# Optimization experiments

Hardware: AMD Instinct MI355X
Metric: run time of the kernel (lower is better)

## Reference

```python
import jax, jax.numpy as jnp
import numpy as np

B, L, C = 8, 4096, 256
H = 8            # num_heads
D = C // H       # head_dim = 32
CHUNK = 128


def _build_slopes(n):
    # ALiBi slopes for power-of-2 n: 2^(-8/n * (i+1)); cast fp16 like the torch module
    s = np.array([2.0 ** (-(8.0 / n) * (i + 1)) for i in range(n)], dtype=np.float32)
    return jnp.asarray(s.astype(np.float16).astype(np.float32))  # [H]


def setup_inputs() -> dict:
    key = jax.random.key(0)
    ks = jax.random.split(key, 6)
    x = jax.random.normal(ks[0], (B, L, C), dtype=jnp.float32)
    rel_pos = jax.random.normal(ks[1], (1, L, C), dtype=jnp.float32) * 0.02  # trunc_normal std=0.02
    qkv_w = jax.random.normal(ks[2], (3 * C, C), dtype=jnp.float32) * (C ** -0.5)
    q_gamma = jnp.ones((H, 1, D), dtype=jnp.float32) / (D ** 0.5)
    k_gamma = jnp.ones((H, 1, D), dtype=jnp.float32) / (D ** 0.5)
    proj_w = jax.random.normal(ks[3], (C, C), dtype=jnp.float32) * (C ** -0.5)
    proj_b = jnp.zeros((C,), dtype=jnp.float32)
    return {"x": x, "rel_pos": rel_pos, "qkv_w": qkv_w, "q_gamma": q_gamma,
            "k_gamma": k_gamma, "proj_w": proj_w, "proj_b": proj_b}


def _rms_norm(t, gamma):
    # t: [B,H,L,D]; gamma: [H,1,D]. F.normalize(dim=-1) then * sqrt(D) * gamma
    n = jnp.sqrt(jnp.sum(t * t, axis=-1, keepdims=True))
    t = t / jnp.maximum(n, 1e-12)
    return t * (D ** 0.5) * gamma[None]


def _lightning_attn(q, k, v, slopes):
    # q,k,v: [B,H,L,D]; slopes: [H]. o_t = sum_{s<=t} exp(-slope*(t-s)) (q_t.k_s) v_s
    nc = L // CHUNK
    c = CHUNK
    qc = q.reshape(B, H, nc, c, D)
    kc = k.reshape(B, H, nc, c, D)
    vc = v.reshape(B, H, nc, c, D)

    idx = jnp.arange(c, dtype=jnp.float32)
    diff = idx[:, None] - idx[None, :]                       # [c,c]
    s = slopes[:, None, None]                                # [H,1,1]
    mask = jnp.where(diff >= 0, jnp.exp(-s * diff), 0.0)     # [H,c,c]

    # intra-chunk: [B,H,nc,c,c]
    scores = jnp.einsum("bhncd,bhnmd->bhncm", qc, kc) * mask[None, :, None]
    o_intra = jnp.einsum("bhncm,bhnmd->bhncd", scores, vc)

    # inter-chunk recurrence over decayed KV state [B,H,D,D]
    q_decay = jnp.exp(-slopes[:, None] * idx[None, :])[None, :, :, None]        # [1,H,c,1]
    k_decay = jnp.exp(-slopes[:, None] * (c - idx[None, :]))[None, :, :, None]  # [1,H,c,1]
    blk_decay = jnp.exp(-slopes * c)[:, None, None]                             # [H,1,1]

    def step(kv, inp):
        qi, ki, vi = inp                                   # each [B,H,c,D]
        o = jnp.einsum("bhcd,bhde->bhce", qi * q_decay, kv)
        kv = blk_decay * kv + jnp.einsum("bhcd,bhce->bhde", ki * k_decay, vi)
        return kv, o

    kv0 = jnp.zeros((B, H, D, D), dtype=q.dtype)
    qs = jnp.moveaxis(qc, 2, 0)  # [nc,B,H,c,D]
    ks_ = jnp.moveaxis(kc, 2, 0)
    vs = jnp.moveaxis(vc, 2, 0)
    _, o_inter = jax.lax.scan(step, kv0, (qs, ks_, vs))    # [nc,B,H,c,D]
    o_inter = jnp.moveaxis(o_inter, 0, 2)                  # [B,H,nc,c,D]

    return (o_intra + o_inter).reshape(B, H, L, D)


def reference(x, rel_pos, qkv_w, q_gamma, k_gamma, proj_w, proj_b):
    slopes = _build_slopes(H)
    h = x + rel_pos                                        # [B,L,C]
    qkv = h @ qkv_w.T                                      # [B,L,3C]
    qkv = qkv.reshape(B, L, 3, H, D).transpose(2, 0, 3, 1, 4)  # [3,B,H,L,D]
    q, k, v = qkv[0], qkv[1], qkv[2]
    q = q * (D ** -0.5)            # no-op through normalize, kept for fidelity
    q = _rms_norm(q, q_gamma)
    k = _rms_norm(k, k_gamma)
    o = _lightning_attn(q, k, v, slopes)                   # [B,H,L,D]
    o = o.transpose(0, 2, 1, 3).reshape(B, L, C)
    return o @ proj_w.T + proj_b
```

## Files before the change

kernel.cpp:

```cpp
#include <hip/hip_runtime.h>
#include <hip/hip_bf16.h>

#define B_ 8
#define L_ 4096
#define C_ 256
#define H_ 8
#define D_ 32
#define CHUNK_ 128
#define NC_ 32
#define M_ (B_*L_)

typedef _Float16 f16x8 __attribute__((ext_vector_type(8)));
typedef _Float16 f16x4 __attribute__((ext_vector_type(4)));
typedef float    f32x4 __attribute__((ext_vector_type(4)));

#define GLOAD_LDS16(g, l) __builtin_amdgcn_global_load_lds( \
    (const __attribute__((address_space(1))) unsigned int*)(g), \
    (__attribute__((address_space(3))) unsigned int*)(l), 16, 0, 0)

__global__ __launch_bounds__(256) void k_cast_w(
    const float* __restrict__ qw, const float* __restrict__ pw,
    _Float16* __restrict__ qwb, _Float16* __restrict__ pwb)
{
    const int i = (blockIdx.x * 256 + threadIdx.x) * 4;
    const float* src; _Float16* dst; int off;
    if (i < 768 * 256) { src = qw; dst = qwb; off = i; }
    else               { src = pw; dst = pwb; off = i - 768 * 256; }
    float4 v = *(const float4*)(src + off);
    f16x4 o = { (_Float16)v.x, (_Float16)v.y, (_Float16)v.z, (_Float16)v.w };
    *(f16x4*)(dst + off) = o;
}

__global__ __launch_bounds__(256) void k_qkv_fused(
    const float* __restrict__ x, const float* __restrict__ rel,
    const _Float16* __restrict__ Bw,
    const float* __restrict__ qg, const float* __restrict__ kg,
    _Float16* __restrict__ Qg, _Float16* __restrict__ Kg, _Float16* __restrict__ Vtg)
{
    __shared__ _Float16 As[128 * 32];
    __shared__ _Float16 Bs[128 * 32];
    __shared__ _Float16 Ws[128 * 132];
    const int tid = threadIdx.x;
    const int wv = tid >> 6, ln = tid & 63;
    const int m0 = blockIdx.y * 128;
    const int n0 = blockIdx.x * 128;
    const int lr = ln >> 2;
    const int lc = (ln & 3) * 8;
    const int wm = (wv >> 1) * 64;
    const int wn = (wv & 1) * 64;
    const int fr = ln & 15;
    const int fk = (ln >> 4) * 8;

    f32x4 acc[4][4] = {};
    const _Float16* gb = Bw + (size_t)(n0 + wv * 16 + lr) * 256 + lc;

    for (int k0 = 0; k0 < 256; k0 += 32) {
        GLOAD_LDS16(gb + k0,            Bs + (wv * 16) * 32);
        GLOAD_LDS16(gb + k0 + 64 * 256, Bs + (64 + wv * 16) * 32);
#pragma unroll
        for (int t = 0; t < 4; ++t) {
            const int flat = t * 256 + tid;
            const int row = flat >> 3;
            const int c4  = (flat & 7) * 4;
            const float* xp = x   + (size_t)(m0 + row) * 256 + k0 + c4;
            const float* rp = rel + (size_t)((m0 + row) & 4095) * 256 + k0 + c4;
            float4 xv = *(const float4*)xp;
            float4 rv = *(const float4*)rp;
            f16x4 hv = { (_Float16)(xv.x + rv.x), (_Float16)(xv.y + rv.y),
                         (_Float16)(xv.z + rv.z), (_Float16)(xv.w + rv.w) };
            *(f16x4*)(As + row * 32 + c4) = hv;
        }
        __syncthreads();
        f16x8 af[4], bf[4];
#pragma unroll
        for (int i = 0; i < 4; ++i)
            af[i] = *(const f16x8*)(As + (wm + i * 16 + fr) * 32 + fk);
#pragma unroll
        for (int j = 0; j < 4; ++j)
            bf[j] = *(const f16x8*)(Bs + (wn + j * 16 + fr) * 32 + fk);
#pragma unroll
        for (int i = 0; i < 4; ++i)
#pragma unroll
            for (int j = 0; j < 4; ++j)
                acc[i][j] = __builtin_amdgcn_mfma_f32_16x16x32_f16(
                    af[i], bf[j], acc[i][j], 0, 0, 0);
        __syncthreads();
    }

    const int cr = (ln >> 4) * 4;
    const int cc = ln & 15;
    const int kind = n0 >> 8;
    const int col0 = (n0 & 255) + wn;
    const int bb   = m0 >> 12;
    const int l00  = m0 & 4095;

    if (kind < 2) {
        const float* gsrc = kind ? kg : qg;
        float gma[2][2];
#pragma unroll
        for (int jp = 0; jp < 2; ++jp)
#pragma unroll
            for (int jj = 0; jj < 2; ++jj)
                gma[jp][jj] = gsrc[((col0 >> 5) + jp) * 32 + jj * 16 + cc];
#pragma unroll
        for (int i = 0; i < 4; ++i)
#pragma unroll
            for (int r = 0; r < 4; ++r) {
                const int irow = wm + i * 16 + cr + r;
#pragma unroll
                for (int jp = 0; jp < 2; ++jp) {
                    const float a0 = acc[i][jp * 2][r];
                    const float a1 = acc[i][jp * 2 + 1][r];
                    float ss = a0 * a0 + a1 * a1;
                    ss += __shfl_xor(ss, 1);
                    ss += __shfl_xor(ss, 2);
                    ss += __shfl_xor(ss, 4);
                    ss += __shfl_xor(ss, 8);
                    const float sc = 5.656854249492381f / fmaxf(sqrtf(ss), 1e-12f);
                    Ws[irow * 132 + wn + jp * 32 + cc]      = (_Float16)(a0 * sc * gma[jp][0]);
                    Ws[irow * 132 + wn + jp * 32 + 16 + cc] = (_Float16)(a1 * sc * gma[jp][1]);
                }
            }
        __syncthreads();
        _Float16* P = kind ? Kg : Qg;
        const int hbase = (n0 & 255) >> 5;
#pragma unroll
        for (int kk = 0; kk < 8; ++kk) {
            const int c = kk * 256 + tid;
            const int hh = c >> 9;
            const int rr = (c >> 2) & 127;
            const int part = (c & 3) * 8;
            f16x8 v8 = *(const f16x8*)(Ws + rr * 132 + hh * 32 + part);
            *(f16x8*)(P + ((size_t)(bb * 8 + hbase + hh) * 4096 + l00 + rr) * 32 + part) = v8;
        }
    } else {
#pragma unroll
        for (int i = 0; i < 4; ++i)
#pragma unroll
            for (int j = 0; j < 4; ++j) {
                const int col = col0 + j * 16 + cc;
                const int hh = col >> 5, e = col & 31;
                const int l0 = l00 + wm + i * 16 + cr;
                f16x4 v4 = { (_Float16)acc[i][j][0], (_Float16)acc[i][j][1],
                             (_Float16)acc[i][j][2], (_Float16)acc[i][j][3] };
                *(f16x4*)(Vtg + ((size_t)(bb * 8 + hh) * 32 + e) * 4096 + l0) = v4;
            }
    }
}

__global__ __launch_bounds__(256) void k_chunk_kv(
    const _Float16* __restrict__ Kg, const _Float16* __restrict__ Vtg,
    float* __restrict__ kvbuf)
{
    __shared__ float ks[128 * 32];
    __shared__ float vst[32 * 129];
    const int blk = blockIdx.x;
    const int n  = blk & 31;
    const int bh = blk >> 5;
    const int h  = bh & 7;
    const float slope = exp2f(-(float)(h + 1));
    const float sl2 = slope * 1.44269504f;
    const int tid = threadIdx.x;
    const _Float16* Kc = Kg + ((size_t)bh * 4096 + n * CHUNK_) * 32;
#pragma unroll
    for (int i = 0; i < 2; ++i) {
        int flat = i * 256 + tid;
        int pos = flat >> 2;
        int d0  = (flat & 3) * 8;
        f16x8 k8 = *(const f16x8*)(Kc + flat * 8);
        float kd = exp2f(-sl2 * (float)(CHUNK_ - pos));
#pragma unroll
        for (int j = 0; j < 8; ++j) ks[pos * 32 + d0 + j] = (float)k8[j] * kd;
        int e = flat >> 4;
        int seg = flat & 15;
        f16x8 v8 = *(const f16x8*)(Vtg + ((size_t)bh * 32 + e) * 4096 + n * CHUNK_ + seg * 8);
#pragma unroll
        for (int j = 0; j < 8; ++j) vst[e * 129 + seg * 8 + j] = (float)v8[j];
    }
    __syncthreads();
    const int e   = tid & 31;
    const int dd0 = tid >> 5;
    float acc[4] = {0.f, 0.f, 0.f, 0.f};
    for (int pos = 0; pos < CHUNK_; ++pos) {
        float vv = vst[e * 129 + pos];
        acc[0] += ks[pos * 32 + dd0 +  0] * vv;
        acc[1] += ks[pos * 32 + dd0 +  8] * vv;
        acc[2] += ks[pos * 32 + dd0 + 16] * vv;
        acc[3] += ks[pos * 32 + dd0 + 24] * vv;
    }
    float* out = kvbuf + (size_t)blk * 1024;
#pragma unroll
    for (int i = 0; i < 4; ++i) out[(dd0 + i * 8) * 32 + e] = acc[i];
}

__global__ __launch_bounds__(256) void k_scan(float* __restrict__ kvbuf)
{
    const int bh = blockIdx.x;
    const int tid = threadIdx.x;
    const float slope = exp2f(-(float)((bh & 7) + 1));
    const float bd = __expf(-slope * (float)CHUNK_);
    float4 st = {0.f, 0.f, 0.f, 0.f};
    float4* base = (float4*)(kvbuf + (size_t)bh * NC_ * 1024) + tid;
#pragma unroll
    for (int g = 0; g < 4; ++g) {
        float4 tmp[8];
#pragma unroll
        for (int k = 0; k < 8; ++k) tmp[k] = base[(g * 8 + k) * 256];
#pragma unroll
        for (int k = 0; k < 8; ++k) {
            base[(g * 8 + k) * 256] = st;
            st.x = bd * st.x + tmp[k].x;
            st.y = bd * st.y + tmp[k].y;
            st.z = bd * st.z + tmp[k].z;
            st.w = bd * st.w + tmp[k].w;
        }
    }
}

__global__ __launch_bounds__(256) void k_attn(
    const _Float16* __restrict__ Qg, const _Float16* __restrict__ Kg,
    const _Float16* __restrict__ Vtg, const float* __restrict__ kvbuf,
    _Float16* __restrict__ attnp)
{
    __shared__ _Float16 Qs[128 * 32];
    __shared__ _Float16 Ks[128 * 32];
    __shared__ _Float16 Vt[32 * 136];
    __shared__ _Float16 KVt[32 * 40];
    __shared__ _Float16 Ss[128 * 136];
    __shared__ _Float16 Os[128 * 36];
    __shared__ float ejs[CHUNK_];
    const int blk = blockIdx.x;
    const int n  = blk & 31;
    const int bh = blk >> 5;
    const int h  = bh & 7;
    const float slope = exp2f(-(float)(h + 1));
    const float sl2 = slope * 1.44269504f;
    const int tid = threadIdx.x;
    const int wv = tid >> 6, ln = tid & 63;

    const _Float16* Qc = Qg + ((size_t)bh * 4096 + n * CHUNK_) * 32;
    const _Float16* Kc = Kg + ((size_t)bh * 4096 + n * CHUNK_) * 32;
#pragma unroll
    for (int i = 0; i < 2; ++i) {
        GLOAD_LDS16(Qc + (wv * 128 + i * 64 + ln) * 8, Qs + (wv * 128 + i * 64) * 8);
        GLOAD_LDS16(Kc + (wv * 128 + i * 64 + ln) * 8, Ks + (wv * 128 + i * 64) * 8);
    }
#pragma unroll
    for (int i = 0; i < 2; ++i) {
        int flat = i * 256 + tid;
        int e = flat >> 4, seg = flat & 15;
        f16x8 v8 = *(const f16x8*)(Vtg + ((size_t)bh * 32 + e) * 4096 + n * CHUNK_ + seg * 8);
        *(f16x8*)(Vt + e * 136 + seg * 8) = v8;
    }
    {
        int e = tid & 31, dg = tid >> 5;
        const float* kvp = kvbuf + (size_t)blk * 1024;
        f16x4 kv4 = { (_Float16)kvp[(dg * 4 + 0) * 32 + e],
                      (_Float16)kvp[(dg * 4 + 1) * 32 + e],
                      (_Float16)kvp[(dg * 4 + 2) * 32 + e],
                      (_Float16)kvp[(dg * 4 + 3) * 32 + e] };
        *(f16x4*)(KVt + e * 40 + dg * 4) = kv4;
    }
    if (tid < CHUNK_) ejs[tid] = exp2f(sl2 * (float)tid);
    __syncthreads();

    const int fr = ln & 15, fk = (ln >> 4) * 8;
    const int cr = (ln >> 4) * 4, cc = ln & 15;

    f16x8 aq[2];
#pragma unroll
    for (int i = 0; i < 2; ++i)
        aq[i] = *(const f16x8*)(Qs + (wv * 32 + i * 16 + fr) * 32 + fk);

    f32x4 sacc[2][8] = {};
#pragma unroll
    for (int j = 0; j < 8; ++j) {
        f16x8 bk = *(const f16x8*)(Ks + (j * 16 + fr) * 32 + fk);
#pragma unroll
        for (int i = 0; i < 2; ++i)
            sacc[i][j] = __builtin_amdgcn_mfma_f32_16x16x32_f16(aq[i], bk, sacc[i][j], 0, 0, 0);
    }
    f32x4 iacc[2][2] = {};
#pragma unroll
    for (int ct = 0; ct < 2; ++ct) {
        f16x8 bkv = *(const f16x8*)(KVt + (ct * 16 + fr) * 40 + fk);
#pragma unroll
        for (int i = 0; i < 2; ++i)
            iacc[i][ct] = __builtin_amdgcn_mfma_f32_16x16x32_f16(aq[i], bkv, iacc[i][ct], 0, 0, 0);
    }
    float ejr[8];
#pragma unroll
    for (int j = 0; j < 8; ++j) ejr[j] = ejs[j * 16 + cc];
    const float c1 = exp2f(-sl2);
    float qd_save[2][4];
#pragma unroll
    for (int i = 0; i < 2; ++i) {
        float er = exp2f(-sl2 * (float)(wv * 32 + i * 16 + cr));
#pragma unroll
        for (int r = 0; r < 4; ++r) {
            const int irow = wv * 32 + i * 16 + cr + r;
            qd_save[i][r] = er;
#pragma unroll
            for (int j = 0; j < 8; ++j) {
                const int jcol = j * 16 + cc;
                const float w = (jcol <= irow) ? ejr[j] * er : 0.f;
                Ss[irow * 136 + jcol] = (_Float16)(sacc[i][j][r] * w);
            }
            er *= c1;
        }
    }
    __syncthreads();

    f32x4 oacc[2][2] = {};
#pragma unroll
    for (int k = 0; k < 4; ++k) {
        f16x8 as[2], bv[2];
#pragma unroll
        for (int i = 0; i < 2; ++i)
            as[i] = *(const f16x8*)(Ss + (wv * 32 + i * 16 + fr) * 136 + k * 32 + fk);
#pragma unroll
        for (int ct = 0; ct < 2; ++ct)
            bv[ct] = *(const f16x8*)(Vt + (ct * 16 + fr) * 136 + k * 32 + fk);
#pragma unroll
        for (int i = 0; i < 2; ++i)
#pragma unroll
            for (int ct = 0; ct < 2; ++ct)
                oacc[i][ct] = __builtin_amdgcn_mfma_f32_16x16x32_f16(as[i], bv[ct], oacc[i][ct], 0, 0, 0);
    }
#pragma unroll
    for (int i = 0; i < 2; ++i)
#pragma unroll
        for (int r = 0; r < 4; ++r) {
            const int irow = wv * 32 + i * 16 + cr + r;
            const float qd = qd_save[i][r];
            Os[irow * 36 + cc]      = (_Float16)(oacc[i][0][r] + qd * iacc[i][0][r]);
            Os[irow * 36 + 16 + cc] = (_Float16)(oacc[i][1][r] + qd * iacc[i][1][r]);
        }
    __syncthreads();
    _Float16* abase = attnp + ((size_t)bh * 4096 + n * CHUNK_) * 32;
#pragma unroll
    for (int kk = 0; kk < 2; ++kk) {
        const int c = kk * 256 + tid;
        const int rr = c >> 2;
        const int part = (c & 3) * 8;
        *(f16x8*)(abase + rr * 32 + part) = *(const f16x8*)(Os + rr * 36 + part);
    }
}

__global__ __launch_bounds__(256) void k_proj_gemm(
    const _Float16* __restrict__ attnp, const _Float16* __restrict__ Bw,
    const float* __restrict__ bias, float* __restrict__ Cc)
{
    __shared__ _Float16 As[128 * 32];
    __shared__ _Float16 Bs[128 * 32];
    const int tid = threadIdx.x;
    const int wv = tid >> 6, ln = tid & 63;
    const int m0 = blockIdx.y * 128;
    const int n0 = blockIdx.x * 128;
    const int lr = ln >> 2;
    const int lc = (ln & 3) * 8;
    const int wm = (wv >> 1) * 64;
    const int wn = (wv & 1) * 64;
    const int fr = ln & 15;
    const int fk = (ln >> 4) * 8;

    f32x4 acc[4][4] = {};
    const int gmrow = m0 + wv * 16 + lr;
    const _Float16* ga = attnp +
        ((size_t)(gmrow >> 12) * 8 * 4096 + (gmrow & 4095)) * 32 + lc;
    const _Float16* gb = Bw + (size_t)(n0 + wv * 16 + lr) * 256 + lc;

    for (int k0 = 0; k0 < 256; k0 += 32) {
        const size_t hoff = (size_t)(k0 >> 5) * (4096 * 32);
        GLOAD_LDS16(ga + hoff,           As + (wv * 16) * 32);
        GLOAD_LDS16(ga + hoff + 64 * 32, As + (64 + wv * 16) * 32);
        GLOAD_LDS16(gb + k0,             Bs + (wv * 16) * 32);
        GLOAD_LDS16(gb + k0 + 64 * 256,  Bs + (64 + wv * 16) * 32);
        __syncthreads();
        f16x8 af[4], bf[4];
#pragma unroll
        for (int i = 0; i < 4; ++i)
            af[i] = *(const f16x8*)(As + (wm + i * 16 + fr) * 32 + fk);
#pragma unroll
        for (int j = 0; j < 4; ++j)
            bf[j] = *(const f16x8*)(Bs + (wn + j * 16 + fr) * 32 + fk);
#pragma unroll
        for (int i = 0; i < 4; ++i)
#pragma unroll
            for (int j = 0; j < 4; ++j)
                acc[i][j] = __builtin_amdgcn_mfma_f32_16x16x32_f16(
                    af[i], bf[j], acc[i][j], 0, 0, 0);
        __syncthreads();
    }
    const int cr = (ln >> 4) * 4;
    const int cc = ln & 15;
#pragma unroll
    for (int i = 0; i < 4; ++i)
#pragma unroll
        for (int j = 0; j < 4; ++j) {
            const int row = m0 + wm + i * 16 + cr;
            const int col = n0 + wn + j * 16 + cc;
            float* cp = Cc + (size_t)row * 256 + col;
            const float bb = bias[col];
#pragma unroll
            for (int r = 0; r < 4; ++r) cp[(size_t)r * 256] = acc[i][j][r] + bb;
        }
}

extern "C" void kernel_launch(void* const* d_in, const int* in_sizes, int n_in,
                              void* d_out, int out_size, void* d_ws, size_t ws_size,
                              hipStream_t stream)
{
    const float* x     = (const float*)d_in[0];
    const float* rel   = (const float*)d_in[1];
    const float* qkv_w = (const float*)d_in[2];
    const float* qg    = (const float*)d_in[3];
    const float* kg    = (const float*)d_in[4];
    const float* pw    = (const float*)d_in[5];
    const float* pb    = (const float*)d_in[6];
    float* out = (float*)d_out;
    char* wsb = (char*)d_ws;

    float*    kvb   = (float*)wsb;
    _Float16* Qg    = (_Float16*)(wsb + ((size_t)8  << 20));
    _Float16* Kg    = (_Float16*)(wsb + ((size_t)24 << 20));
    _Float16* Vtg   = (_Float16*)(wsb + ((size_t)40 << 20));
    _Float16* attnp = (_Float16*)(wsb + ((size_t)56 << 20));
    _Float16* qwb   = (_Float16*)(wsb + ((size_t)72 << 20));
    _Float16* pwb   = (_Float16*)(wsb + ((size_t)73 << 20));

    k_cast_w<<<256, 256, 0, stream>>>(qkv_w, pw, qwb, pwb);
    k_qkv_fused<<<dim3(6, 256), 256, 0, stream>>>(x, rel, qwb, qg, kg, Qg, Kg, Vtg);
    k_chunk_kv<<<2048, 256, 0, stream>>>(Kg, Vtg, kvb);
    k_scan<<<64, 256, 0, stream>>>(kvb);
    k_attn<<<2048, 256, 0, stream>>>(Qg, Kg, Vtg, kvb, attnp);
    k_proj_gemm<<<dim3(2, 256), 256, 0, stream>>>(attnp, pwb, pb, out);
}
```

Baseline: 204.9 us.

## Widen QKV GEMM tile to 128x256 with 512 threads, revectorize chunk KV

The QKV projection kernel now computes a full 256-column slice (one of q/k/v) per block with 8 waves, so each x+rel tile is loaded and converted once per kind instead of twice. Shared memory is aliased between the staging buffers and the output staging buffer, and the normalized output is written one head pair at a time with extra barriers. The chunk KV kernel transposes V in LDS so each thread accumulates a float4 of outputs with vector LDS reads and a vector store. The risks are the extra syncs in the epilogue and possible register pressure at 512 threads.

```diff
diff --git a/kernel.cpp b/kernel.cpp
--- a/kernel.cpp
+++ b/kernel.cpp
@@ -31,116 +31,110 @@
     *(f16x4*)(dst + off) = o;
 }
 
-__global__ __launch_bounds__(256) void k_qkv_fused(
+__global__ __launch_bounds__(512) void k_qkv_fused(
     const float* __restrict__ x, const float* __restrict__ rel,
     const _Float16* __restrict__ Bw,
     const float* __restrict__ qg, const float* __restrict__ kg,
     _Float16* __restrict__ Qg, _Float16* __restrict__ Kg, _Float16* __restrict__ Vtg)
 {
-    __shared__ _Float16 As[128 * 32];
-    __shared__ _Float16 Bs[128 * 32];
-    __shared__ _Float16 Ws[128 * 132];
+    __shared__ __align__(16) char smem[24576];
+    _Float16* As = (_Float16*)smem;
+    _Float16* Bs = As + 128 * 32;
+    _Float16* Ws = (_Float16*)smem;
+
     const int tid = threadIdx.x;
     const int wv = tid >> 6, ln = tid & 63;
+    const int kind = blockIdx.x;
     const int m0 = blockIdx.y * 128;
-    const int n0 = blockIdx.x * 128;
-    const int lr = ln >> 2;
-    const int lc = (ln & 3) * 8;
-    const int wm = (wv >> 1) * 64;
-    const int wn = (wv & 1) * 64;
-    const int fr = ln & 15;
-    const int fk = (ln >> 4) * 8;
-
-    f32x4 acc[4][4] = {};
-    const _Float16* gb = Bw + (size_t)(n0 + wv * 16 + lr) * 256 + lc;
-
+    const int wr = wv >> 1, wc = wv & 1;
+    const int lr = ln >> 2, lc = (ln & 3) * 8;
+    const int fr = ln & 15, fk = (ln >> 4) * 8;
+
+    const int arow = tid >> 2;
+    const int aseg = (tid & 3) * 8;
+    const float* xp = x   + (size_t)(m0 + arow) * 256 + aseg;
+    const float* rp = rel + (size_t)((m0 + arow) & 4095) * 256 + aseg;
+    const _Float16* gb = Bw + (size_t)(kind * 256 + wv * 16 + lr) * 256 + lc;
+
+    f32x4 acc[2][8] = {};
     for (int k0 = 0; k0 < 256; k0 += 32) {
-        GLOAD_LDS16(gb + k0,            Bs + (wv * 16) * 32);
-        GLOAD_LDS16(gb + k0 + 64 * 256, Bs + (64 + wv * 16) * 32);
-#pragma unroll
-        for (int t = 0; t < 4; ++t) {
-            const int flat = t * 256 + tid;
-            const int row = flat >> 3;
-            const int c4  = (flat & 7) * 4;
-            const float* xp = x   + (size_t)(m0 + row) * 256 + k0 + c4;
-            const float* rp = rel + (size_t)((m0 + row) & 4095) * 256 + k0 + c4;
-            float4 xv = *(const float4*)xp;
-            float4 rv = *(const float4*)rp;
-            f16x4 hv = { (_Float16)(xv.x + rv.x), (_Float16)(xv.y + rv.y),
-                         (_Float16)(xv.z + rv.z), (_Float16)(xv.w + rv.w) };
-            *(f16x4*)(As + row * 32 + c4) = hv;
-        }
+        GLOAD_LDS16(gb + k0,             Bs + (wv * 16) * 32);
+        GLOAD_LDS16(gb + k0 + 128 * 256, Bs + (128 + wv * 16) * 32);
+        float4 x0 = *(const float4*)(xp + k0);
+        float4 x1 = *(const float4*)(xp + k0 + 4);
+        float4 r0 = *(const float4*)(rp + k0);
+        float4 r1 = *(const float4*)(rp + k0 + 4);
+        f16x8 hv = { (_Float16)(x0.x + r0.x), (_Float16)(x0.y + r0.y),
+                     (_Float16)(x0.z + r0.z), (_Float16)(x0.w + r0.w),
+                     (_Float16)(x1.x + r1.x), (_Float16)(x1.y + r1.y),
+                     (_Float16)(x1.z + r1.z), (_Float16)(x1.w + r1.w) };
+        *(f16x8*)(As + arow * 32 + aseg) = hv;
         __syncthreads();
-        f16x8 af[4], bf[4];
-#pragma unroll
-        for (int i = 0; i < 4; ++i)
-            af[i] = *(const f16x8*)(As + (wm + i * 16 + fr) * 32 + fk);
-#pragma unroll
-        for (int j = 0; j < 4; ++j)
-            bf[j] = *(const f16x8*)(Bs + (wn + j * 16 + fr) * 32 + fk);
-#pragma unroll
-        for (int i = 0; i < 4; ++i)
-#pragma unroll
-            for (int j = 0; j < 4; ++j)
+        f16x8 af[2], bf[8];
+#pragma unroll
+        for (int i = 0; i < 2; ++i)
+            af[i] = *(const f16x8*)(As + (wr * 32 + i * 16 + fr) * 32 + fk);
+#pragma unroll
+        for (int j = 0; j < 8; ++j)
+            bf[j] = *(const f16x8*)(Bs + (wc * 128 + j * 16 + fr) * 32 + fk);
+#pragma unroll
+        for (int i = 0; i < 2; ++i)
+#pragma unroll
+            for (int j = 0; j < 8; ++j)
                 acc[i][j] = __builtin_amdgcn_mfma_f32_16x16x32_f16(
                     af[i], bf[j], acc[i][j], 0, 0, 0);
         __syncthreads();
     }
 
-    const int cr = (ln >> 4) * 4;
-    const int cc = ln & 15;
-    const int kind = n0 >> 8;
-    const int col0 = (n0 & 255) + wn;
-    const int bb   = m0 >> 12;
-    const int l00  = m0 & 4095;
+    const int cr = (ln >> 4) * 4, cc = ln & 15;
+    const int bb = m0 >> 12, l00 = m0 & 4095;
 
     if (kind < 2) {
         const float* gsrc = kind ? kg : qg;
-        float gma[2][2];
-#pragma unroll
-        for (int jp = 0; jp < 2; ++jp)
-#pragma unroll
-            for (int jj = 0; jj < 2; ++jj)
-                gma[jp][jj] = gsrc[((col0 >> 5) + jp) * 32 + jj * 16 + cc];
-#pragma unroll
-        for (int i = 0; i < 4; ++i)
-#pragma unroll
-            for (int r = 0; r < 4; ++r) {
-                const int irow = wm + i * 16 + cr + r;
-#pragma unroll
-                for (int jp = 0; jp < 2; ++jp) {
-                    const float a0 = acc[i][jp * 2][r];
-                    const float a1 = acc[i][jp * 2 + 1][r];
+        _Float16* P = kind ? Kg : Qg;
+#pragma unroll
+        for (int p = 0; p < 4; ++p) {
+            const int h = wc * 4 + p;
+            const float g0 = gsrc[h * 32 + cc];
+            const float g1 = gsrc[h * 32 + 16 + cc];
+#pragma unroll
+            for (int i = 0; i < 2; ++i)
+#pragma unroll
+                for (int r = 0; r < 4; ++r) {
+                    const float a0 = acc[i][2 * p][r];
+                    const float a1 = acc[i][2 * p + 1][r];
                     float ss = a0 * a0 + a1 * a1;
                     ss += __shfl_xor(ss, 1);
                     ss += __shfl_xor(ss, 2);
                     ss += __shfl_xor(ss, 4);
                     ss += __shfl_xor(ss, 8);
                     const float sc = 5.656854249492381f / fmaxf(sqrtf(ss), 1e-12f);
-                    Ws[irow * 132 + wn + jp * 32 + cc]      = (_Float16)(a0 * sc * gma[jp][0]);
-                    Ws[irow * 132 + wn + jp * 32 + 16 + cc] = (_Float16)(a1 * sc * gma[jp][1]);
+                    const int row = wr * 32 + i * 16 + cr + r;
+                    Ws[row * 72 + wc * 32 + cc]      = (_Float16)(a0 * sc * g0);
+                    Ws[row * 72 + wc * 32 + 16 + cc] = (_Float16)(a1 * sc * g1);
                 }
+            __syncthreads();
+            const int half = tid >> 8;
+            const int t = tid & 255;
+            const int hh = half * 4 + p;
+            _Float16* dst = P + ((size_t)(bb * 8 + hh) * 4096 + l00) * 32;
+#pragma unroll
+            for (int cidx = 0; cidx < 2; ++cidx) {
+                const int c = t + cidx * 256;
+                const int rr = c >> 2, part = (c & 3) * 8;
+                f16x8 v8 = *(const f16x8*)(Ws + rr * 72 + half * 32 + part);
+                *(f16x8*)(dst + rr * 32 + part) = v8;
             }
-        __syncthreads();
-        _Float16* P = kind ? Kg : Qg;
-        const int hbase = (n0 & 255) >> 5;
-#pragma unroll
-        for (int kk = 0; kk < 8; ++kk) {
-            const int c = kk * 256 + tid;
-            const int hh = c >> 9;
-            const int rr = (c >> 2) & 127;
-            const int part = (c & 3) * 8;
-            f16x8 v8 = *(const f16x8*)(Ws + rr * 132 + hh * 32 + part);
-            *(f16x8*)(P + ((size_t)(bb * 8 + hbase + hh) * 4096 + l00 + rr) * 32 + part) = v8;
+            __syncthreads();
         }
     } else {
 #pragma unroll
-        for (int i = 0; i < 4; ++i)
-#pragma unroll
-            for (int j = 0; j < 4; ++j) {
-                const int col = col0 + j * 16 + cc;
+        for (int i = 0; i < 2; ++i)
+#pragma unroll
+            for (int j = 0; j < 8; ++j) {
+                const int col = wc * 128 + j * 16 + cc;
                 const int hh = col >> 5, e = col & 31;
-                const int l0 = l00 + wm + i * 16 + cr;
+                const int l0 = l00 + wr * 32 + i * 16 + cr;
                 f16x4 v4 = { (_Float16)acc[i][j][0], (_Float16)acc[i][j][1],
                              (_Float16)acc[i][j][2], (_Float16)acc[i][j][3] };
                 *(f16x4*)(Vtg + ((size_t)(bb * 8 + hh) * 32 + e) * 4096 + l0) = v4;
@@ -153,44 +147,39 @@
     float* __restrict__ kvbuf)
 {
     __shared__ float ks[128 * 32];
-    __shared__ float vst[32 * 129];
+    __shared__ float vs[128 * 36];
     const int blk = blockIdx.x;
     const int n  = blk & 31;
     const int bh = blk >> 5;
     const int h  = bh & 7;
-    const float slope = exp2f(-(float)(h + 1));
-    const float sl2 = slope * 1.44269504f;
+    const float sl2 = exp2f(-(float)(h + 1)) * 1.44269504f;
     const int tid = threadIdx.x;
     const _Float16* Kc = Kg + ((size_t)bh * 4096 + n * CHUNK_) * 32;
 #pragma unroll
     for (int i = 0; i < 2; ++i) {
-        int flat = i * 256 + tid;
-        int pos = flat >> 2;
-        int d0  = (flat & 3) * 8;
+        const int flat = i * 256 + tid;
+        const int pos = flat >> 2, d0 = (flat & 3) * 8;
         f16x8 k8 = *(const f16x8*)(Kc + flat * 8);
-        float kd = exp2f(-sl2 * (float)(CHUNK_ - pos));
-#pragma unroll
-        for (int j = 0; j < 8; ++j) ks[pos * 32 + d0 + j] = (float)k8[j] * kd;
-        int e = flat >> 4;
-        int seg = flat & 15;
+        const float kd = exp2f(-sl2 * (float)(CHUNK_ - pos));
+        f32x4 lo = { (float)k8[0] * kd, (float)k8[1] * kd, (float)k8[2] * kd, (float)k8[3] * kd };
+        f32x4 hi = { (float)k8[4] * kd, (float)k8[5] * kd, (float)k8[6] * kd, (float)k8[7] * kd };
+        *(f32x4*)&ks[pos * 32 + d0]     = lo;
+        *(f32x4*)&ks[pos * 32 + d0 + 4] = hi;
+        const int e = flat >> 4, seg = flat & 15;
         f16x8 v8 = *(const f16x8*)(Vtg + ((size_t)bh * 32 + e) * 4096 + n * CHUNK_ + seg * 8);
 #pragma unroll
-        for (int j = 0; j < 8; ++j) vst[e * 129 + seg * 8 + j] = (float)v8[j];
+        for (int j = 0; j < 8; ++j) vs[(seg * 8 + j) * 36 + e] = (float)v8[j];
     }
     __syncthreads();
-    const int e   = tid & 31;
-    const int dd0 = tid >> 5;
-    float acc[4] = {0.f, 0.f, 0.f, 0.f};
+    const int d = tid >> 3;
+    const int e0 = (tid & 7) * 4;
+    f32x4 acc = {0.f, 0.f, 0.f, 0.f};
     for (int pos = 0; pos < CHUNK_; ++pos) {
-        float vv = vst[e * 129 + pos];
-        acc[0] += ks[pos * 32 + dd0 +  0] * vv;
-        acc[1] += ks[pos * 32 + dd0 +  8] * vv;
-        acc[2] += ks[pos * 32 + dd0 + 16] * vv;
-        acc[3] += ks[pos * 32 + dd0 + 24] * vv;
-    }
-    float* out = kvbuf + (size_t)blk * 1024;
-#pragma unroll
-    for (int i = 0; i < 4; ++i) out[(dd0 + i * 8) * 32 + e] = acc[i];
+        const float kd = ks[pos * 32 + d];
+        f32x4 v4 = *(const f32x4*)&vs[pos * 36 + e0];
+        acc += kd * v4;
+    }
+    *(f32x4*)(kvbuf + (size_t)blk * 1024 + d * 32 + e0) = acc;
 }
 
 __global__ __launch_bounds__(256) void k_scan(float* __restrict__ kvbuf)
@@ -233,8 +222,7 @@
     const int n  = blk & 31;
     const int bh = blk >> 5;
     const int h  = bh & 7;
-    const float slope = exp2f(-(float)(h + 1));
-    const float sl2 = slope * 1.44269504f;
+    const float sl2 = exp2f(-(float)(h + 1)) * 1.44269504f;
     const int tid = threadIdx.x;
     const int wv = tid >> 6, ln = tid & 63;
 
@@ -430,7 +418,7 @@
     _Float16* pwb   = (_Float16*)(wsb + ((size_t)73 << 20));
 
     k_cast_w<<<256, 256, 0, stream>>>(qkv_w, pw, qwb, pwb);
-    k_qkv_fused<<<dim3(6, 256), 256, 0, stream>>>(x, rel, qwb, qg, kg, Qg, Kg, Vtg);
+    k_qkv_fused<<<dim3(3, 256), 512, 0, stream>>>(x, rel, qwb, qg, kg, Qg, Kg, Vtg);
     k_chunk_kv<<<2048, 256, 0, stream>>>(Kg, Vtg, kvb);
     k_scan<<<64, 256, 0, stream>>>(kvb);
     k_attn<<<2048, 256, 0, stream>>>(Qg, Kg, Vtg, kvb, attnp);
```

After: 203.4 us. No clear change (-0.8%).
